# Kernel optimization log

Measured on AMD Instinct MI355X. Metric: run time of the kernel, lower is better.

The kernel has to match this reference:

```python
import jax, jax.numpy as jnp
import numpy as np

EPS_BN = 1e-3   # nn.BatchNorm1d(eps=0.001)
LAMDA = 1e-5    # Point_Attentation.lamda


def _bn(x, g, b, m, v):
    # inference-mode BatchNorm1d over last dim
    return (x - m) * (g * jax.lax.rsqrt(v + EPS_BN)) + b


def _forward(features_low, features_high,
             bott_W, bott_b, bott_gamma, bott_beta, bott_mean, bott_var,
             qkv_W, qkv_gamma, qkv_beta, qkv_mean, qkv_var,
             mlp_W, mlp_gamma, mlp_beta, mlp_mean, mlp_var,
             fus_W, fus_b, fus_gamma, fus_beta, fus_mean, fus_var,
             batch_size):
    N, C = features_low.shape
    B = batch_size
    n = N // B  # points per batch segment (equal-length segments)

    # ---- Point_Attentation: per-point channel mean, var over channels / (n-1) ----
    x = features_low
    mean = jnp.mean(x, axis=-1, keepdims=True)
    d = x - mean
    var = jnp.sum(d * d, axis=-1, keepdims=True) / (n - 1)
    e_t = d * d / (4.0 * (var + LAMDA)) + 0.5
    x = x + jax.nn.sigmoid(e_t) * x

    for i in range(3):
        y = jax.nn.relu(_bn(x @ bott_W[2 * i] + bott_b[2 * i],
                            bott_gamma[2 * i], bott_beta[2 * i], bott_mean[2 * i], bott_var[2 * i]))
        y = jax.nn.relu(_bn(y @ bott_W[2 * i + 1] + bott_b[2 * i + 1],
                            bott_gamma[2 * i + 1], bott_beta[2 * i + 1], bott_mean[2 * i + 1], bott_var[2 * i + 1]))
        x = x + y

    # ---- fusion: per-batch QKV attention between low (x) and high features ----
    low = x.reshape(B, n, C)
    high = features_high.reshape(B, n, C)

    q = _bn(jnp.einsum('bnc,cd->bnd', low, qkv_W[0]), qkv_gamma[0], qkv_beta[0], qkv_mean[0], qkv_var[0])
    k = _bn(jnp.einsum('bnc,cd->bnd', high, qkv_W[1]), qkv_gamma[1], qkv_beta[1], qkv_mean[1], qkv_var[1])
    v = _bn(jnp.einsum('bnc,cd->bnd', high, qkv_W[2]), qkv_gamma[2], qkv_beta[2], qkv_mean[2], qkv_var[2])

    scale = 1.0 / jnp.sqrt(jnp.asarray(256.0, dtype=q.dtype))  # normal_dim = 256
    attn = jax.nn.softmax(jnp.einsum('bqc,bkc->bqk', q, k) * scale, axis=-1)
    ao = jnp.einsum('bqk,bkc->bqc', attn, v)

    # mlp: (Linear no-bias -> BN -> Dropout(eval=id) -> ReLU) x2
    h = jax.nn.relu(_bn(jnp.einsum('bnc,cd->bnd', ao, mlp_W[0]), mlp_gamma[0], mlp_beta[0], mlp_mean[0], mlp_var[0]))
    h = jax.nn.relu(_bn(jnp.einsum('bnc,cd->bnd', h, mlp_W[1]), mlp_gamma[1], mlp_beta[1], mlp_mean[1], mlp_var[1]))

    # linear_fusion: Linear(2C->C, bias) -> BN -> ReLU
    cat = jnp.concatenate([low, h], axis=-1)  # [B, n, 2C]
    out = jax.nn.relu(_bn(jnp.einsum('bnc,cd->bnd', cat, fus_W) + fus_b, fus_gamma, fus_beta, fus_mean, fus_var))
    return out.reshape(N, C)


def setup_inputs() -> dict:
    key = jax.random.key(0)
    ks = jax.random.split(key, 16)
    N, C, B = 16384, 256, 4
    s = 0.05
    d = {}
    d['features_low'] = jax.random.normal(ks[0], (N, C), jnp.float32)
    d['features_high'] = jax.random.normal(ks[1], (N, C), jnp.float32)
    d['bott_W'] = jax.random.normal(ks[2], (6, C, C), jnp.float32) * s
    d['bott_b'] = jnp.zeros((6, C), jnp.float32)
    d['bott_gamma'] = jnp.ones((6, C), jnp.float32)
    d['bott_beta'] = jnp.zeros((6, C), jnp.float32)
    d['bott_mean'] = jnp.zeros((6, C), jnp.float32)
    d['bott_var'] = jnp.ones((6, C), jnp.float32)
    d['qkv_W'] = jax.random.normal(ks[3], (3, C, C), jnp.float32) * s
    d['qkv_gamma'] = jnp.ones((3, C), jnp.float32)
    d['qkv_beta'] = jnp.zeros((3, C), jnp.float32)
    d['qkv_mean'] = jnp.zeros((3, C), jnp.float32)
    d['qkv_var'] = jnp.ones((3, C), jnp.float32)
    d['mlp_W'] = jax.random.normal(ks[4], (2, C, C), jnp.float32) * s
    d['mlp_gamma'] = jnp.ones((2, C), jnp.float32)
    d['mlp_beta'] = jnp.zeros((2, C), jnp.float32)
    d['mlp_mean'] = jnp.zeros((2, C), jnp.float32)
    d['mlp_var'] = jnp.ones((2, C), jnp.float32)
    d['fus_W'] = jax.random.normal(ks[5], (2 * C, C), jnp.float32) * s
    d['fus_b'] = jnp.zeros((C,), jnp.float32)
    d['fus_gamma'] = jnp.ones((C,), jnp.float32)
    d['fus_beta'] = jnp.zeros((C,), jnp.float32)
    d['fus_mean'] = jnp.zeros((C,), jnp.float32)
    d['fus_var'] = jnp.ones((C,), jnp.float32)
    d['batch_size'] = B
    return d


def reference(features_low, features_high,
              bott_W, bott_b, bott_gamma, bott_beta, bott_mean, bott_var,
              qkv_W, qkv_gamma, qkv_beta, qkv_mean, qkv_var,
              mlp_W, mlp_gamma, mlp_beta, mlp_mean, mlp_var,
              fus_W, fus_b, fus_gamma, fus_beta, fus_mean, fus_var,
              batch_size):
    return _forward(features_low, features_high,
                    bott_W, bott_b, bott_gamma, bott_beta, bott_mean, bott_var,
                    qkv_W, qkv_gamma, qkv_beta, qkv_mean, qkv_var,
                    mlp_W, mlp_gamma, mlp_beta, mlp_mean, mlp_var,
                    fus_W, fus_b, fus_gamma, fus_beta, fus_mean, fus_var,
                    batch_size)
```

## Files before the change

kernel.cpp:

```cpp
#include <hip/hip_runtime.h>
#include <cstdint>
#include <cstddef>

typedef float v4f __attribute__((ext_vector_type(4)));
typedef float v2f __attribute__((ext_vector_type(2)));
typedef short v8s __attribute__((ext_vector_type(8)));
typedef unsigned short v4u __attribute__((ext_vector_type(4)));

typedef unsigned short ubf;

#define NPTS 16384
#define CD   256
#define NBAT 4
#define NPB  4096

__device__ __forceinline__ float bf2f(ubf u) {
    union { unsigned u; float f; } c; c.u = ((unsigned)u) << 16; return c.f;
}
__device__ __forceinline__ ubf f2bf(float f) {
    union { float f; unsigned u; } c; c.f = f;
    unsigned u = c.u;
    u += 0x7fffu + ((u >> 16) & 1u);
    return (ubf)(u >> 16);
}

__global__ __launch_bounds__(256) void k_pre(
    const float* __restrict__ low, float* __restrict__ xout,
    const float* __restrict__ bott, const float* __restrict__ qkv,
    const float* __restrict__ mlp, const float* __restrict__ fus,
    ubf* __restrict__ wt) {
    const int bid = blockIdx.x;
    if (bid < 4096) {
        const int lane = threadIdx.x & 63;
        const int row  = bid * 4 + (threadIdx.x >> 6);
        const float* p = low + (size_t)row * CD + lane * 4;
        v4f v = *reinterpret_cast<const v4f*>(p);
        float d[4];
        float s = v[0] + v[1] + v[2] + v[3];
#pragma unroll
        for (int o = 32; o >= 1; o >>= 1) s += __shfl_xor(s, o);
        const float mean = s * (1.0f / 256.0f);
        float ss = 0.f;
#pragma unroll
        for (int i = 0; i < 4; ++i) { d[i] = v[i] - mean; ss += d[i] * d[i]; }
#pragma unroll
        for (int o = 32; o >= 1; o >>= 1) ss += __shfl_xor(ss, o);
        const float var = ss * (1.0f / 4095.0f);
        const float dn  = 1.0f / (4.0f * (var + 1e-5f));
        v4f o;
#pragma unroll
        for (int i = 0; i < 4; ++i) {
            const float e   = d[i] * d[i] * dn + 0.5f;
            const float sig = 1.0f / (1.0f + __expf(-e));
            o[i] = v[i] * (1.0f + sig);
        }
        *reinterpret_cast<v4f*>(xout + (size_t)row * CD + lane * 4) = o;
        return;
    }
    const int bid2 = bid - 4096;
    const int z = bid2 >> 7, r = bid2 & 127;
    const float* src; int K; size_t doff;
    if (z < 6)       { src = bott + (size_t)z * 65536;       K = 256; doff = (size_t)z * 65536; }
    else if (z < 9)  { src = qkv  + (size_t)(z - 6) * 65536; K = 256; doff = (size_t)z * 65536; }
    else if (z < 11) { src = mlp  + (size_t)(z - 9) * 65536; K = 256; doff = (size_t)z * 65536; }
    else             { src = fus;                            K = 512; doff = (size_t)11 * 65536; }
    const int kt = (r >> 3) * 32, nt = (r & 7) * 32;
    if (kt >= K) return;
    __shared__ ubf tile[32][33];
    const int tx = threadIdx.x & 31, ty = threadIdx.x >> 5;
#pragma unroll
    for (int i = 0; i < 4; ++i)
        tile[ty * 4 + i][tx] = f2bf(src[(size_t)(kt + ty * 4 + i) * 256 + nt + tx]);
    __syncthreads();
    ubf* dst = wt + doff;
#pragma unroll
    for (int i = 0; i < 4; ++i)
        dst[(size_t)(nt + ty * 4 + i) * K + kt + tx] = tile[tx][ty * 4 + i];
}

__global__ __launch_bounds__(256) void k_conv1(
    float* __restrict__ xA, const ubf* __restrict__ wT,
    const float* __restrict__ bb, const float* __restrict__ bg,
    const float* __restrict__ bbe, const float* __restrict__ bm_,
    const float* __restrict__ bv) {
    __shared__ __attribute__((aligned(16))) float xls[64 * 256];
    __shared__ __attribute__((aligned(16))) ubf   yls[64 * 256];

    const int lane = threadIdx.x & 63;
    const int w    = threadIdx.x >> 6;
    const int wr = w >> 1, wc = w & 1;
    const int q15 = lane & 15, g = lane >> 4;
    const int bm = blockIdx.x * 64;

    {
        float* xsrcb = xA + (size_t)bm * 256;
#pragma unroll
        for (int it = 0; it < 16; ++it) {
            const int L4 = (it * 256 + w * 64) * 4;
            const int Ll = L4 + lane * 4;
            const int row = Ll >> 8, col = (Ll & 255) ^ ((row & 7) << 3);
            __builtin_amdgcn_global_load_lds(
                (const __attribute__((address_space(1))) unsigned*)(xsrcb + row * 256 + col),
                (__attribute__((address_space(3))) unsigned*)(xls + L4), 16, 0, 0);
        }
    }
    __syncthreads();

    const int r0l = wr * 32 + q15;
#pragma unroll 1
    for (int s = 0; s < 3; ++s) {
        const ubf* W0 = wT + (size_t)(2 * s) * 65536;
        const ubf* W1 = wT + (size_t)(2 * s + 1) * 65536;

        v4f acc[2][8];
#pragma unroll
        for (int i = 0; i < 2; ++i)
#pragma unroll
            for (int j = 0; j < 8; ++j)
#pragma unroll
                for (int r = 0; r < 4; ++r) acc[i][j][r] = 0.f;
        for (int ks = 0; ks < 8; ++ks) {
            const int k0 = ks * 32 + g * 8;
            v8s afr[2], bfr[8];
#pragma unroll
            for (int mi = 0; mi < 2; ++mi) {
                const int row = r0l + mi * 16;
                const float* ap = &xls[row * 256 + (k0 ^ ((row & 7) << 3))];
                v4f a = *reinterpret_cast<const v4f*>(ap);
                v4f b = *reinterpret_cast<const v4f*>(ap + 4);
                v8s t;
#pragma unroll
                for (int j = 0; j < 4; ++j) { t[j] = (short)f2bf(a[j]); t[j + 4] = (short)f2bf(b[j]); }
                afr[mi] = t;
            }
#pragma unroll
            for (int ni = 0; ni < 8; ++ni)
                bfr[ni] = *reinterpret_cast<const v8s*>(W0 + (size_t)(wc * 128 + ni * 16 + q15) * 256 + k0);
#pragma unroll
            for (int mi = 0; mi < 2; ++mi)
#pragma unroll
                for (int ni = 0; ni < 8; ++ni)
                    acc[mi][ni] = __builtin_amdgcn_mfma_f32_16x16x32_bf16(afr[mi], bfr[ni], acc[mi][ni], 0, 0, 0);
        }
#pragma unroll
        for (int ni = 0; ni < 8; ++ni) {
            const int col = wc * 128 + ni * 16 + q15;
            const float sc  = bg[2 * s * 256 + col] * rsqrtf(bv[2 * s * 256 + col] + 1e-3f);
            const float tc  = bbe[2 * s * 256 + col] - bm_[2 * s * 256 + col] * sc;
            const float bia = bb[2 * s * 256 + col];
#pragma unroll
            for (int mi = 0; mi < 2; ++mi)
#pragma unroll
                for (int r = 0; r < 4; ++r) {
                    const int row = wr * 32 + mi * 16 + g * 4 + r;
                    float z = fmaxf((acc[mi][ni][r] + bia) * sc + tc, 0.f);
                    yls[row * 256 + (col ^ ((row & 7) << 3))] = f2bf(z);
                }
        }
        __syncthreads();

#pragma unroll
        for (int i = 0; i < 2; ++i)
#pragma unroll
            for (int j = 0; j < 8; ++j)
#pragma unroll
                for (int r = 0; r < 4; ++r) acc[i][j][r] = 0.f;
        for (int ks = 0; ks < 8; ++ks) {
            const int k0 = ks * 32 + g * 8;
            v8s afr[2], bfr[8];
#pragma unroll
            for (int mi = 0; mi < 2; ++mi) {
                const int row = r0l + mi * 16;
                afr[mi] = *reinterpret_cast<const v8s*>(&yls[row * 256 + (k0 ^ ((row & 7) << 3))]);
            }
#pragma unroll
            for (int ni = 0; ni < 8; ++ni)
                bfr[ni] = *reinterpret_cast<const v8s*>(W1 + (size_t)(wc * 128 + ni * 16 + q15) * 256 + k0);
#pragma unroll
            for (int mi = 0; mi < 2; ++mi)
#pragma unroll
                for (int ni = 0; ni < 8; ++ni)
                    acc[mi][ni] = __builtin_amdgcn_mfma_f32_16x16x32_bf16(afr[mi], bfr[ni], acc[mi][ni], 0, 0, 0);
        }
#pragma unroll
        for (int ni = 0; ni < 8; ++ni) {
            const int col = wc * 128 + ni * 16 + q15;
            const int c1 = (2 * s + 1) * 256 + col;
            const float sc  = bg[c1] * rsqrtf(bv[c1] + 1e-3f);
            const float tc  = bbe[c1] - bm_[c1] * sc;
            const float bia = bb[c1];
#pragma unroll
            for (int mi = 0; mi < 2; ++mi)
#pragma unroll
                for (int r = 0; r < 4; ++r) {
                    const int row = wr * 32 + mi * 16 + g * 4 + r;
                    float z = fmaxf((acc[mi][ni][r] + bia) * sc + tc, 0.f);
                    xls[row * 256 + (col ^ ((row & 7) << 3))] += z;
                }
        }
        __syncthreads();
    }

    {
        float* xdstb = xA + (size_t)bm * 256;
#pragma unroll
        for (int it = 0; it < 16; ++it) {
            const int Ll = (it * 256 + threadIdx.x) * 4;
            const int row = Ll >> 8, cl = Ll & 255;
            const int gcol = cl ^ ((row & 7) << 3);
            *reinterpret_cast<v4f*>(xdstb + row * 256 + gcol) =
                *reinterpret_cast<const v4f*>(xls + Ll);
        }
    }
}

__global__ __launch_bounds__(256) void k_qkv(
    const float* __restrict__ xA, const float* __restrict__ fh,
    const ubf* __restrict__ wTq,
    const float* __restrict__ qg, const float* __restrict__ qbe,
    const float* __restrict__ qm, const float* __restrict__ qv,
    ubf* __restrict__ qB, ubf* __restrict__ kB, ubf* __restrict__ vT) {
    const int m = blockIdx.y >> 1;
    const float* Af = (m == 0) ? xA : fh;
    const ubf* WT = wTq + m * 65536;
    const float* gamma = qg + m * 256;
    const float* beta  = qbe + m * 256;
    const float* bmean = qm + m * 256;
    const float* bvar  = qv + m * 256;

    const int lane = threadIdx.x & 63;
    const int w    = threadIdx.x >> 6;
    const int wr = w >> 1, wc = w & 1;
    const int q15 = lane & 15, g = lane >> 4;
    const int bm = blockIdx.x * 128, bn = (blockIdx.y & 1) * 128;
    const int r0 = bm + wr * 64 + q15;
    const int c0 = bn + wc * 64 + q15;

    v4f acc[4][4];
#pragma unroll
    for (int i = 0; i < 4; ++i)
#pragma unroll
        for (int j = 0; j < 4; ++j)
#pragma unroll
            for (int r = 0; r < 4; ++r) acc[i][j][r] = 0.f;

    for (int ks = 0; ks < 8; ++ks) {
        const int k0 = ks * 32 + g * 8;
        v8s afr[4], bfr[4];
#pragma unroll
        for (int mi = 0; mi < 4; ++mi) {
            const float* ap = Af + (size_t)(r0 + mi * 16) * CD + k0;
            v4f a = *reinterpret_cast<const v4f*>(ap);
            v4f b = *reinterpret_cast<const v4f*>(ap + 4);
            v8s t;
#pragma unroll
            for (int j = 0; j < 4; ++j) { t[j] = (short)f2bf(a[j]); t[j + 4] = (short)f2bf(b[j]); }
            afr[mi] = t;
        }
#pragma unroll
        for (int ni = 0; ni < 4; ++ni)
            bfr[ni] = *reinterpret_cast<const v8s*>(WT + (size_t)(c0 + ni * 16) * 256 + k0);
#pragma unroll
        for (int mi = 0; mi < 4; ++mi)
#pragma unroll
            for (int ni = 0; ni < 4; ++ni)
                acc[mi][ni] = __builtin_amdgcn_mfma_f32_16x16x32_bf16(afr[mi], bfr[ni], acc[mi][ni], 0, 0, 0);
    }

    ubf* outb = (m == 0) ? qB : kB;
#pragma unroll
    for (int ni = 0; ni < 4; ++ni) {
        const int col = c0 + ni * 16;
        const float sc = gamma[col] * rsqrtf(bvar[col] + 1e-3f);
        const float tc = beta[col] - bmean[col] * sc;
#pragma unroll
        for (int mi = 0; mi < 4; ++mi) {
            if (m == 2) {
                const int row0 = bm + wr * 64 + mi * 16 + g * 4;
                v4u pk;
#pragma unroll
                for (int r = 0; r < 4; ++r) pk[r] = f2bf(acc[mi][ni][r] * sc + tc);
                const int bb = row0 >> 12, key = row0 & 4095;
                *reinterpret_cast<v4u*>(vT + ((size_t)(bb * CD + col)) * NPB + key) = pk;
            } else {
#pragma unroll
                for (int r = 0; r < 4; ++r) {
                    const int row = bm + wr * 64 + mi * 16 + g * 4 + r;
                    outb[(size_t)row * CD + col] = f2bf(acc[mi][ni][r] * sc + tc);
                }
            }
        }
    }
}

__device__ __forceinline__ void stage_k32(const ubf* __restrict__ kg,
                                          ubf* kd, int wave, int lane) {
#pragma unroll
    for (int it = 0; it < 8; ++it) {
        const int Lb = it * 1024 + wave * 512;
        const int L  = Lb + lane * 8;
        const int key = L >> 8, c8 = (L & 255) ^ ((key & 7) << 3);
        __builtin_amdgcn_global_load_lds(
            (const __attribute__((address_space(1))) unsigned*)(kg + key * CD + c8),
            (__attribute__((address_space(3))) unsigned*)(kd + Lb), 16, 0, 0);
    }
}
__device__ __forceinline__ void stage_v32(const ubf* __restrict__ vg,
                                          ubf* vd, int wave, int lane) {
#pragma unroll
    for (int it = 0; it < 8; ++it) {
        const int Lb = it * 1024 + wave * 512;
        const int L  = Lb + lane * 8;
        const int cpair = L >> 6;
        const int rem   = (L & 63) ^ ((cpair & 7) << 3);
        const int c = cpair * 2 + (rem >> 5), k = rem & 31;
        __builtin_amdgcn_global_load_lds(
            (const __attribute__((address_space(1))) unsigned*)(vg + (size_t)c * NPB + k),
            (__attribute__((address_space(3))) unsigned*)(vd + Lb), 16, 0, 0);
    }
}

__global__ __launch_bounds__(128, 2) void k_attn(const ubf* __restrict__ qb, const ubf* __restrict__ kb,
                                                 const ubf* __restrict__ vt,
                                                 ubf* __restrict__ o0, ubf* __restrict__ o1,
                                                 float* __restrict__ ml) {
    __shared__ __attribute__((aligned(16))) ubf kls[32 * 256];
    __shared__ __attribute__((aligned(16))) ubf vls[128 * 64];
    __shared__ __attribute__((aligned(16))) ubf pls[2 * 1024];

    const int raw = blockIdx.x;
    const int xcd = raw & 7, qt = raw >> 3;
    const int b = xcd >> 1, half = xcd & 1;

    const int wave = threadIdx.x >> 6, lane = threadIdx.x & 63;
    const int q15 = lane & 15, g = lane >> 4;
    const int swzP = (q15 & 7) << 3;

    const ubf* qrow = qb + ((size_t)(b * NPB + qt * 32 + wave * 16 + q15)) * CD + g * 8;
    v8s qf[8];
#pragma unroll
    for (int cs = 0; cs < 8; ++cs) qf[cs] = *reinterpret_cast<const v8s*>(qrow + cs * 32);

    v4f oacc[16];
#pragma unroll
    for (int i = 0; i < 16; ++i)
#pragma unroll
        for (int r = 0; r < 4; ++r) oacc[i][r] = 0.f;
    float m_run = -3.0e38f, l_run = 0.f;

    const ubf* kgb = kb + ((size_t)(b * NPB) + half * 2048) * CD;
    const ubf* vgb = vt + (size_t)b * CD * NPB + half * 2048;
    ubf* pw = pls + wave * 1024;

    stage_k32(kgb, kls, wave, lane);
    stage_v32(vgb, vls, wave, lane);
    __syncthreads();

    for (int kc = 0; kc < 64; ++kc) {
        v4f sacc[2];
#pragma unroll
        for (int f = 0; f < 2; ++f)
#pragma unroll
            for (int r = 0; r < 4; ++r) sacc[f][r] = 0.f;
#pragma unroll
        for (int cs = 0; cs < 8; ++cs)
#pragma unroll
            for (int f = 0; f < 2; ++f) {
                const int key = 16 * f + q15;
                v8s af = *reinterpret_cast<const v8s*>(&kls[(key * CD + cs * 32 + g * 8) ^ ((key & 7) << 3)]);
                sacc[f] = __builtin_amdgcn_mfma_f32_16x16x32_bf16(af, qf[cs], sacc[f], 0, 0, 0);
            }

        __syncthreads();
        if (kc + 1 < 64)
            stage_k32(kgb + (size_t)(kc + 1) * 32 * CD, kls, wave, lane);

        float mloc = -3.0e38f;
#pragma unroll
        for (int f = 0; f < 2; ++f)
#pragma unroll
            for (int r = 0; r < 4; ++r) {
                float x = sacc[f][r] * 0.0625f;
                sacc[f][r] = x;
                mloc = fmaxf(mloc, x);
            }
        mloc = fmaxf(mloc, __shfl_xor(mloc, 16));
        mloc = fmaxf(mloc, __shfl_xor(mloc, 32));
        if (!__all(mloc <= m_run + 8.0f)) {
            const float mnew  = fmaxf(m_run, mloc);
            const float alpha = __expf(m_run - mnew);
            l_run *= alpha;
#pragma unroll
            for (int i = 0; i < 16; ++i)
#pragma unroll
                for (int r = 0; r < 4; ++r) oacc[i][r] *= alpha;
            m_run = mnew;
        }
        float lloc = 0.f;
#pragma unroll
        for (int f = 0; f < 2; ++f)
#pragma unroll
            for (int r = 0; r < 4; ++r) {
                float p = __expf(sacc[f][r] - m_run);
                sacc[f][r] = p;
                lloc += p;
            }
        lloc += __shfl_xor(lloc, 16);
        lloc += __shfl_xor(lloc, 32);
        l_run += lloc;

#pragma unroll
        for (int f = 0; f < 2; ++f) {
            unsigned u0, u1, u2, u3;
            { union { float f; unsigned u; } c; c.f = sacc[f][0]; u0 = c.u; }
            { union { float f; unsigned u; } c; c.f = sacc[f][1]; u1 = c.u; }
            { union { float f; unsigned u; } c; c.f = sacc[f][2]; u2 = c.u; }
            { union { float f; unsigned u; } c; c.f = sacc[f][3]; u3 = c.u; }
            unsigned p01 = (u0 >> 16) | (u1 & 0xFFFF0000u);
            unsigned p23 = (u2 >> 16) | (u3 & 0xFFFF0000u);
            const int e = q15 * 64 + 16 * f + 4 * g;
            *reinterpret_cast<unsigned*>(&pw[(e)     ^ swzP]) = p01;
            *reinterpret_cast<unsigned*>(&pw[(e + 2) ^ swzP]) = p23;
        }
        v8s pb = *reinterpret_cast<const v8s*>(&pw[(q15 * 64 + 8 * g) ^ swzP]);
#pragma unroll
        for (int mt = 0; mt < 16; ++mt) {
            const int cp = 8 * mt + (q15 >> 1);
            const int e  = cp * 64 + ((((q15 & 1) << 5) | (g << 3)) ^ ((q15 >> 1) << 3));
            v8s av = *reinterpret_cast<const v8s*>(&vls[e]);
            oacc[mt] = __builtin_amdgcn_mfma_f32_16x16x32_bf16(av, pb, oacc[mt], 0, 0, 0);
        }

        __syncthreads();
        if (kc + 1 < 64)
            stage_v32(vgb + (kc + 1) * 32, vls, wave, lane);
    }

    const int grow = b * NPB + qt * 32 + wave * 16 + q15;
    ubf* aor = (half ? o1 : o0) + (size_t)grow * CD;
#pragma unroll
    for (int mt = 0; mt < 16; ++mt) {
        v4u pk;
#pragma unroll
        for (int r = 0; r < 4; ++r) pk[r] = f2bf(oacc[mt][r]);
        *reinterpret_cast<v4u*>(aor + 16 * mt + 4 * g) = pk;
    }
    if (g == 0) {
        v2f d; d[0] = m_run; d[1] = l_run;
        *reinterpret_cast<v2f*>(ml + (size_t)(half * NPTS + grow) * 2) = d;
    }
}

__global__ __launch_bounds__(256) void k_tail(
    const ubf* __restrict__ o0, const ubf* __restrict__ o1, const float* __restrict__ ml,
    const float* __restrict__ xA, const ubf* __restrict__ wT,
    const float* __restrict__ mg, const float* __restrict__ mbe,
    const float* __restrict__ mm, const float* __restrict__ mv,
    const float* __restrict__ fb, const float* __restrict__ fg,
    const float* __restrict__ fbe, const float* __restrict__ fm,
    const float* __restrict__ fv, float* __restrict__ out) {
    __shared__ __attribute__((aligned(16))) ubf yls[64 * 256];

    const int lane = threadIdx.x & 63;
    const int w    = threadIdx.x >> 6;
    const int wr = w >> 1, wc = w & 1;
    const int q15 = lane & 15, g = lane >> 4;
    const int bm = blockIdx.x * 64;
    const int r0l = wr * 32 + q15;

    const ubf* W9  = wT + (size_t)9 * 65536;
    const ubf* W10 = wT + (size_t)10 * 65536;
    const ubf* W11 = wT + (size_t)11 * 65536;

    v4f acc[2][8];

    float a0[2], a1[2];
#pragma unroll
    for (int mi = 0; mi < 2; ++mi) {
        const int row = bm + r0l + mi * 16;
        const float m0 = ml[2 * row],          l0 = ml[2 * row + 1];
        const float m1 = ml[2 * (NPTS + row)], l1 = ml[2 * (NPTS + row) + 1];
        const float mx = fmaxf(m0, m1);
        const float w0 = __expf(m0 - mx), w1 = __expf(m1 - mx);
        const float inv = 1.0f / (w0 * l0 + w1 * l1);
        a0[mi] = w0 * inv; a1[mi] = w1 * inv;
    }
#pragma unroll
    for (int i = 0; i < 2; ++i)
#pragma unroll
        for (int j = 0; j < 8; ++j)
#pragma unroll
            for (int r = 0; r < 4; ++r) acc[i][j][r] = 0.f;
    for (int ks = 0; ks < 8; ++ks) {
        const int k0 = ks * 32 + g * 8;
        v8s afr[2], bfr[8];
#pragma unroll
        for (int mi = 0; mi < 2; ++mi) {
            const int row = bm + r0l + mi * 16;
            v8s u0 = *reinterpret_cast<const v8s*>(o0 + (size_t)row * CD + k0);
            v8s u1 = *reinterpret_cast<const v8s*>(o1 + (size_t)row * CD + k0);
            v8s t;
#pragma unroll
            for (int j = 0; j < 8; ++j)
                t[j] = (short)f2bf(a0[mi] * bf2f((ubf)u0[j]) + a1[mi] * bf2f((ubf)u1[j]));
            afr[mi] = t;
        }
#pragma unroll
        for (int ni = 0; ni < 8; ++ni)
            bfr[ni] = *reinterpret_cast<const v8s*>(W9 + (size_t)(wc * 128 + ni * 16 + q15) * 256 + k0);
#pragma unroll
        for (int mi = 0; mi < 2; ++mi)
#pragma unroll
            for (int ni = 0; ni < 8; ++ni)
                acc[mi][ni] = __builtin_amdgcn_mfma_f32_16x16x32_bf16(afr[mi], bfr[ni], acc[mi][ni], 0, 0, 0);
    }
#pragma unroll
    for (int ni = 0; ni < 8; ++ni) {
        const int col = wc * 128 + ni * 16 + q15;
        const float sc = mg[col] * rsqrtf(mv[col] + 1e-3f);
        const float tc = mbe[col] - mm[col] * sc;
#pragma unroll
        for (int mi = 0; mi < 2; ++mi)
#pragma unroll
            for (int r = 0; r < 4; ++r) {
                const int row = wr * 32 + mi * 16 + g * 4 + r;
                float z = fmaxf(acc[mi][ni][r] * sc + tc, 0.f);
                yls[row * 256 + (col ^ ((row & 7) << 3))] = f2bf(z);
            }
    }
    __syncthreads();

#pragma unroll
    for (int i = 0; i < 2; ++i)
#pragma unroll
        for (int j = 0; j < 8; ++j)
#pragma unroll
            for (int r = 0; r < 4; ++r) acc[i][j][r] = 0.f;
    for (int ks = 0; ks < 8; ++ks) {
        const int k0 = ks * 32 + g * 8;
        v8s afr[2], bfr[8];
#pragma unroll
        for (int mi = 0; mi < 2; ++mi) {
            const int row = r0l + mi * 16;
            afr[mi] = *reinterpret_cast<const v8s*>(&yls[row * 256 + (k0 ^ ((row & 7) << 3))]);
        }
#pragma unroll
        for (int ni = 0; ni < 8; ++ni)
            bfr[ni] = *reinterpret_cast<const v8s*>(W10 + (size_t)(wc * 128 + ni * 16 + q15) * 256 + k0);
#pragma unroll
        for (int mi = 0; mi < 2; ++mi)
#pragma unroll
            for (int ni = 0; ni < 8; ++ni)
                acc[mi][ni] = __builtin_amdgcn_mfma_f32_16x16x32_bf16(afr[mi], bfr[ni], acc[mi][ni], 0, 0, 0);
    }
    __syncthreads();
#pragma unroll
    for (int ni = 0; ni < 8; ++ni) {
        const int col = wc * 128 + ni * 16 + q15;
        const float sc = mg[256 + col] * rsqrtf(mv[256 + col] + 1e-3f);
        const float tc = mbe[256 + col] - mm[256 + col] * sc;
#pragma unroll
        for (int mi = 0; mi < 2; ++mi)
#pragma unroll
            for (int r = 0; r < 4; ++r) {
                const int row = wr * 32 + mi * 16 + g * 4 + r;
                float z = fmaxf(acc[mi][ni][r] * sc + tc, 0.f);
                yls[row * 256 + (col ^ ((row & 7) << 3))] = f2bf(z);
            }
    }
    __syncthreads();

#pragma unroll
    for (int i = 0; i < 2; ++i)
#pragma unroll
        for (int j = 0; j < 8; ++j)
#pragma unroll
            for (int r = 0; r < 4; ++r) acc[i][j][r] = 0.f;
    for (int ks = 0; ks < 16; ++ks) {
        const int k0 = ks * 32 + g * 8;
        v8s afr[2], bfr[8];
#pragma unroll
        for (int mi = 0; mi < 2; ++mi) {
            if (k0 < 256) {
                const float* ap = xA + (size_t)(bm + r0l + mi * 16) * CD + k0;
                v4f a = *reinterpret_cast<const v4f*>(ap);
                v4f b = *reinterpret_cast<const v4f*>(ap + 4);
                v8s t;
#pragma unroll
                for (int j = 0; j < 4; ++j) { t[j] = (short)f2bf(a[j]); t[j + 4] = (short)f2bf(b[j]); }
                afr[mi] = t;
            } else {
                const int row = r0l + mi * 16, kk = k0 - 256;
                afr[mi] = *reinterpret_cast<const v8s*>(&yls[row * 256 + (kk ^ ((row & 7) << 3))]);
            }
        }
#pragma unroll
        for (int ni = 0; ni < 8; ++ni)
            bfr[ni] = *reinterpret_cast<const v8s*>(W11 + (size_t)(wc * 128 + ni * 16 + q15) * 512 + k0);
#pragma unroll
        for (int mi = 0; mi < 2; ++mi)
#pragma unroll
            for (int ni = 0; ni < 8; ++ni)
                acc[mi][ni] = __builtin_amdgcn_mfma_f32_16x16x32_bf16(afr[mi], bfr[ni], acc[mi][ni], 0, 0, 0);
    }
#pragma unroll
    for (int ni = 0; ni < 8; ++ni) {
        const int col = wc * 128 + ni * 16 + q15;
        const float sc = fg[col] * rsqrtf(fv[col] + 1e-3f);
        const float tc = fbe[col] - fm[col] * sc;
        const float bia = fb[col];
#pragma unroll
        for (int mi = 0; mi < 2; ++mi)
#pragma unroll
            for (int r = 0; r < 4; ++r) {
                const int row = bm + wr * 32 + mi * 16 + g * 4 + r;
                float z = fmaxf((acc[mi][ni][r] + bia) * sc + tc, 0.f);
                out[(size_t)row * CD + col] = z;
            }
    }
}

extern "C" void kernel_launch(void* const* d_in, const int* in_sizes, int n_in,
                              void* d_out, int out_size, void* d_ws, size_t ws_size,
                              hipStream_t stream) {
    const float* f_low   = (const float*)d_in[0];
    const float* f_high  = (const float*)d_in[1];
    const float* bott_W  = (const float*)d_in[2];
    const float* bott_b  = (const float*)d_in[3];
    const float* bott_g  = (const float*)d_in[4];
    const float* bott_be = (const float*)d_in[5];
    const float* bott_m  = (const float*)d_in[6];
    const float* bott_v  = (const float*)d_in[7];
    const float* qkv_W   = (const float*)d_in[8];
    const float* qkv_g   = (const float*)d_in[9];
    const float* qkv_be  = (const float*)d_in[10];
    const float* qkv_m   = (const float*)d_in[11];
    const float* qkv_v   = (const float*)d_in[12];
    const float* mlp_W   = (const float*)d_in[13];
    const float* mlp_g   = (const float*)d_in[14];
    const float* mlp_be  = (const float*)d_in[15];
    const float* mlp_m   = (const float*)d_in[16];
    const float* mlp_v   = (const float*)d_in[17];
    const float* fus_W   = (const float*)d_in[18];
    const float* fus_b   = (const float*)d_in[19];
    const float* fus_g   = (const float*)d_in[20];
    const float* fus_be  = (const float*)d_in[21];
    const float* fus_m   = (const float*)d_in[22];
    const float* fus_v   = (const float*)d_in[23];
    (void)in_sizes; (void)n_in; (void)out_size; (void)ws_size;

    char* ws = (char*)d_ws;
    const size_t MB = 1024 * 1024;
    float* xA = (float*)(ws);
    ubf*   o0 = (ubf*)  (ws + 17 * MB);
    ubf*   qB = (ubf*)  (ws + 26 * MB);
    ubf*   kB = (ubf*)  (ws + 35 * MB);
    ubf*   vT = (ubf*)  (ws + 44 * MB);
    ubf*   wT = (ubf*)  (ws + 53 * MB);
    ubf*   o1 = (ubf*)  (ws + 56 * MB);
    float* ml = (float*)(ws + 65 * MB);

    k_pre<<<dim3(4096 + 1536), dim3(256), 0, stream>>>(f_low, xA,
                                                       bott_W, qkv_W, mlp_W, fus_W, wT);

    k_conv1<<<dim3(256), dim3(256), 0, stream>>>(xA, wT,
                                                 bott_b, bott_g, bott_be, bott_m, bott_v);

    k_qkv<<<dim3(128, 6), dim3(256), 0, stream>>>(xA, f_high, wT + (size_t)6 * 65536,
                                                  qkv_g, qkv_be, qkv_m, qkv_v, qB, kB, vT);

    k_attn<<<dim3(1024), dim3(128), 0, stream>>>(qB, kB, vT, o0, o1, ml);

    k_tail<<<dim3(256), dim3(256), 0, stream>>>(o0, o1, ml, xA, wT,
                                                mlp_g, mlp_be, mlp_m, mlp_v,
                                                fus_b, fus_g, fus_be, fus_m, fus_v,
                                                (float*)d_out);
}
```

Before: 305.5 us.

## Switch attention kernel to 32x32x16 MFMA with 64-query tiles and chunked V layout

The flash-attention kernel now uses 32x32x16 bf16 MFMAs with each wave handling 32 queries, so each block covers 64 queries and the grid is halved. This doubles reuse of each staged K/V chunk and cuts K/V LDS traffic per query. V is written in a key-chunked layout (32 keys per channel row) and staged into LDS with a padded 40-element row stride instead of XOR swizzling, and P uses the same padding. The accumulators grow to 128 registers per lane and launch bounds drop to one block per SIMD hint, which lowers occupancy. The padding entries are filled by loading from a dummy address.

```diff
diff --git a/kernel.cpp b/kernel.cpp
--- a/kernel.cpp
+++ b/kernel.cpp
@@ -4,6 +4,7 @@
 
 typedef float v4f __attribute__((ext_vector_type(4)));
 typedef float v2f __attribute__((ext_vector_type(2)));
+typedef float v16f __attribute__((ext_vector_type(16)));
 typedef short v8s __attribute__((ext_vector_type(8)));
 typedef unsigned short v4u __attribute__((ext_vector_type(4)));
 
@@ -281,7 +282,9 @@
 #pragma unroll
                 for (int r = 0; r < 4; ++r) pk[r] = f2bf(acc[mi][ni][r] * sc + tc);
                 const int bb = row0 >> 12, key = row0 & 4095;
-                *reinterpret_cast<v4u*>(vT + ((size_t)(bb * CD + col)) * NPB + key) = pk;
+                const int ch = key >> 5, kin = key & 31;
+                *reinterpret_cast<v4u*>(vT + (size_t)bb * (CD * NPB)
+                                           + (size_t)ch * (CD * 32) + col * 32 + kin) = pk;
             } else {
 #pragma unroll
                 for (int r = 0; r < 4; ++r) {
@@ -305,71 +308,66 @@
             (__attribute__((address_space(3))) unsigned*)(kd + Lb), 16, 0, 0);
     }
 }
-__device__ __forceinline__ void stage_v32(const ubf* __restrict__ vg,
+__device__ __forceinline__ void stage_v40(const ubf* __restrict__ vchunk,
                                           ubf* vd, int wave, int lane) {
 #pragma unroll
-    for (int it = 0; it < 8; ++it) {
-        const int Lb = it * 1024 + wave * 512;
-        const int L  = Lb + lane * 8;
-        const int cpair = L >> 6;
-        const int rem   = (L & 63) ^ ((cpair & 7) << 3);
-        const int c = cpair * 2 + (rem >> 5), k = rem & 31;
+    for (int it = 0; it < 10; ++it) {
+        const int e0b = wave * 5120 + it * 512;
+        const int e0  = e0b + lane * 8;
+        const int c   = e0 / 40;
+        const int k0  = e0 - c * 40;
+        const ubf* src = (k0 < 32) ? (vchunk + c * 32 + k0) : vchunk;
         __builtin_amdgcn_global_load_lds(
-            (const __attribute__((address_space(1))) unsigned*)(vg + (size_t)c * NPB + k),
-            (__attribute__((address_space(3))) unsigned*)(vd + Lb), 16, 0, 0);
-    }
-}
-
-__global__ __launch_bounds__(128, 2) void k_attn(const ubf* __restrict__ qb, const ubf* __restrict__ kb,
+            (const __attribute__((address_space(1))) unsigned*)src,
+            (__attribute__((address_space(3))) unsigned*)(vd + e0b), 16, 0, 0);
+    }
+}
+
+__global__ __launch_bounds__(128, 1) void k_attn(const ubf* __restrict__ qb, const ubf* __restrict__ kb,
                                                  const ubf* __restrict__ vt,
                                                  ubf* __restrict__ o0, ubf* __restrict__ o1,
                                                  float* __restrict__ ml) {
     __shared__ __attribute__((aligned(16))) ubf kls[32 * 256];
-    __shared__ __attribute__((aligned(16))) ubf vls[128 * 64];
-    __shared__ __attribute__((aligned(16))) ubf pls[2 * 1024];
+    __shared__ __attribute__((aligned(16))) ubf vls[256 * 40];
+    __shared__ __attribute__((aligned(16))) ubf pls[2 * 32 * 40];
 
     const int raw = blockIdx.x;
     const int xcd = raw & 7, qt = raw >> 3;
     const int b = xcd >> 1, half = xcd & 1;
 
     const int wave = threadIdx.x >> 6, lane = threadIdx.x & 63;
-    const int q15 = lane & 15, g = lane >> 4;
-    const int swzP = (q15 & 7) << 3;
-
-    const ubf* qrow = qb + ((size_t)(b * NPB + qt * 32 + wave * 16 + q15)) * CD + g * 8;
-    v8s qf[8];
-#pragma unroll
-    for (int cs = 0; cs < 8; ++cs) qf[cs] = *reinterpret_cast<const v8s*>(qrow + cs * 32);
-
-    v4f oacc[16];
-#pragma unroll
-    for (int i = 0; i < 16; ++i)
-#pragma unroll
-        for (int r = 0; r < 4; ++r) oacc[i][r] = 0.f;
+    const int q31 = lane & 31, h = lane >> 5;
+
+    const ubf* qrow = qb + ((size_t)(b * NPB + qt * 64 + wave * 32 + q31)) * CD + h * 8;
+    v8s qf[16];
+#pragma unroll
+    for (int ks = 0; ks < 16; ++ks) qf[ks] = *reinterpret_cast<const v8s*>(qrow + ks * 16);
+
+    v16f oacc[8];
+#pragma unroll
+    for (int t = 0; t < 8; ++t)
+#pragma unroll
+        for (int r = 0; r < 16; ++r) oacc[t][r] = 0.f;
     float m_run = -3.0e38f, l_run = 0.f;
 
     const ubf* kgb = kb + ((size_t)(b * NPB) + half * 2048) * CD;
-    const ubf* vgb = vt + (size_t)b * CD * NPB + half * 2048;
-    ubf* pw = pls + wave * 1024;
+    const ubf* vgb = vt + (size_t)b * (CD * NPB) + (size_t)(half * 64) * (CD * 32);
+    ubf* pw = pls + wave * (32 * 40);
 
     stage_k32(kgb, kls, wave, lane);
-    stage_v32(vgb, vls, wave, lane);
+    stage_v40(vgb, vls, wave, lane);
     __syncthreads();
 
     for (int kc = 0; kc < 64; ++kc) {
-        v4f sacc[2];
-#pragma unroll
-        for (int f = 0; f < 2; ++f)
-#pragma unroll
-            for (int r = 0; r < 4; ++r) sacc[f][r] = 0.f;
-#pragma unroll
-        for (int cs = 0; cs < 8; ++cs)
-#pragma unroll
-            for (int f = 0; f < 2; ++f) {
-                const int key = 16 * f + q15;
-                v8s af = *reinterpret_cast<const v8s*>(&kls[(key * CD + cs * 32 + g * 8) ^ ((key & 7) << 3)]);
-                sacc[f] = __builtin_amdgcn_mfma_f32_16x16x32_bf16(af, qf[cs], sacc[f], 0, 0, 0);
-            }
+        v16f sacc;
+#pragma unroll
+        for (int r = 0; r < 16; ++r) sacc[r] = 0.f;
+#pragma unroll
+        for (int ks = 0; ks < 16; ++ks) {
+            v8s af = *reinterpret_cast<const v8s*>(
+                &kls[q31 * 256 + ((ks * 16 + h * 8) ^ ((q31 & 7) << 3))]);
+            sacc = __builtin_amdgcn_mfma_f32_32x32x16_bf16(af, qf[ks], sacc, 0, 0, 0);
+        }
 
         __syncthreads();
         if (kc + 1 < 64)
@@ -377,75 +375,73 @@
 
         float mloc = -3.0e38f;
 #pragma unroll
-        for (int f = 0; f < 2; ++f)
-#pragma unroll
-            for (int r = 0; r < 4; ++r) {
-                float x = sacc[f][r] * 0.0625f;
-                sacc[f][r] = x;
-                mloc = fmaxf(mloc, x);
-            }
-        mloc = fmaxf(mloc, __shfl_xor(mloc, 16));
+        for (int r = 0; r < 16; ++r) {
+            float x = sacc[r] * 0.0625f;
+            sacc[r] = x;
+            mloc = fmaxf(mloc, x);
+        }
         mloc = fmaxf(mloc, __shfl_xor(mloc, 32));
         if (!__all(mloc <= m_run + 8.0f)) {
             const float mnew  = fmaxf(m_run, mloc);
             const float alpha = __expf(m_run - mnew);
             l_run *= alpha;
 #pragma unroll
-            for (int i = 0; i < 16; ++i)
-#pragma unroll
-                for (int r = 0; r < 4; ++r) oacc[i][r] *= alpha;
+            for (int t = 0; t < 8; ++t)
+#pragma unroll
+                for (int r = 0; r < 16; ++r) oacc[t][r] *= alpha;
             m_run = mnew;
         }
         float lloc = 0.f;
 #pragma unroll
-        for (int f = 0; f < 2; ++f)
-#pragma unroll
-            for (int r = 0; r < 4; ++r) {
-                float p = __expf(sacc[f][r] - m_run);
-                sacc[f][r] = p;
-                lloc += p;
-            }
-        lloc += __shfl_xor(lloc, 16);
+        for (int r = 0; r < 16; ++r) {
+            float p = __expf(sacc[r] - m_run);
+            sacc[r] = p;
+            lloc += p;
+        }
         lloc += __shfl_xor(lloc, 32);
         l_run += lloc;
 
 #pragma unroll
-        for (int f = 0; f < 2; ++f) {
+        for (int G = 0; G < 4; ++G) {
             unsigned u0, u1, u2, u3;
-            { union { float f; unsigned u; } c; c.f = sacc[f][0]; u0 = c.u; }
-            { union { float f; unsigned u; } c; c.f = sacc[f][1]; u1 = c.u; }
-            { union { float f; unsigned u; } c; c.f = sacc[f][2]; u2 = c.u; }
-            { union { float f; unsigned u; } c; c.f = sacc[f][3]; u3 = c.u; }
+            { union { float f; unsigned u; } c; c.f = sacc[4 * G + 0]; u0 = c.u; }
+            { union { float f; unsigned u; } c; c.f = sacc[4 * G + 1]; u1 = c.u; }
+            { union { float f; unsigned u; } c; c.f = sacc[4 * G + 2]; u2 = c.u; }
+            { union { float f; unsigned u; } c; c.f = sacc[4 * G + 3]; u3 = c.u; }
             unsigned p01 = (u0 >> 16) | (u1 & 0xFFFF0000u);
             unsigned p23 = (u2 >> 16) | (u3 & 0xFFFF0000u);
-            const int e = q15 * 64 + 16 * f + 4 * g;
-            *reinterpret_cast<unsigned*>(&pw[(e)     ^ swzP]) = p01;
-            *reinterpret_cast<unsigned*>(&pw[(e + 2) ^ swzP]) = p23;
-        }
-        v8s pb = *reinterpret_cast<const v8s*>(&pw[(q15 * 64 + 8 * g) ^ swzP]);
-#pragma unroll
-        for (int mt = 0; mt < 16; ++mt) {
-            const int cp = 8 * mt + (q15 >> 1);
-            const int e  = cp * 64 + ((((q15 & 1) << 5) | (g << 3)) ^ ((q15 >> 1) << 3));
-            v8s av = *reinterpret_cast<const v8s*>(&vls[e]);
-            oacc[mt] = __builtin_amdgcn_mfma_f32_16x16x32_bf16(av, pb, oacc[mt], 0, 0, 0);
+            const int e = q31 * 40 + 8 * G + 4 * h;
+            *reinterpret_cast<unsigned*>(&pw[e])     = p01;
+            *reinterpret_cast<unsigned*>(&pw[e + 2]) = p23;
+        }
+        v8s pb0 = *reinterpret_cast<const v8s*>(&pw[q31 * 40 + 0  + 8 * h]);
+        v8s pb1 = *reinterpret_cast<const v8s*>(&pw[q31 * 40 + 16 + 8 * h]);
+#pragma unroll
+        for (int t = 0; t < 8; ++t) {
+            const int crow = (t * 32 + q31) * 40;
+            v8s av0 = *reinterpret_cast<const v8s*>(&vls[crow + 0  + 8 * h]);
+            oacc[t] = __builtin_amdgcn_mfma_f32_32x32x16_bf16(av0, pb0, oacc[t], 0, 0, 0);
+            v8s av1 = *reinterpret_cast<const v8s*>(&vls[crow + 16 + 8 * h]);
+            oacc[t] = __builtin_amdgcn_mfma_f32_32x32x16_bf16(av1, pb1, oacc[t], 0, 0, 0);
         }
 
         __syncthreads();
         if (kc + 1 < 64)
-            stage_v32(vgb + (kc + 1) * 32, vls, wave, lane);
-    }
-
-    const int grow = b * NPB + qt * 32 + wave * 16 + q15;
+            stage_v40(vgb + (size_t)(kc + 1) * (CD * 32), vls, wave, lane);
+    }
+
+    const int grow = b * NPB + qt * 64 + wave * 32 + q31;
     ubf* aor = (half ? o1 : o0) + (size_t)grow * CD;
 #pragma unroll
-    for (int mt = 0; mt < 16; ++mt) {
-        v4u pk;
-#pragma unroll
-        for (int r = 0; r < 4; ++r) pk[r] = f2bf(oacc[mt][r]);
-        *reinterpret_cast<v4u*>(aor + 16 * mt + 4 * g) = pk;
-    }
-    if (g == 0) {
+    for (int t = 0; t < 8; ++t)
+#pragma unroll
+        for (int G = 0; G < 4; ++G) {
+            v4u pk;
+#pragma unroll
+            for (int r = 0; r < 4; ++r) pk[r] = f2bf(oacc[t][4 * G + r]);
+            *reinterpret_cast<v4u*>(aor + t * 32 + 8 * G + 4 * h) = pk;
+        }
+    if (h == 0) {
         v2f d; d[0] = m_run; d[1] = l_run;
         *reinterpret_cast<v2f*>(ml + (size_t)(half * NPTS + grow) * 2) = d;
     }
@@ -669,7 +665,7 @@
     k_qkv<<<dim3(128, 6), dim3(256), 0, stream>>>(xA, f_high, wT + (size_t)6 * 65536,
                                                   qkv_g, qkv_be, qkv_m, qkv_v, qB, kB, vT);
 
-    k_attn<<<dim3(1024), dim3(128), 0, stream>>>(qB, kB, vT, o0, o1, ml);
+    k_attn<<<dim3(512), dim3(128), 0, stream>>>(qB, kB, vT, o0, o1, ml);
 
     k_tail<<<dim3(256), dim3(256), 0, stream>>>(o0, o1, ml, xA, wT,
                                                 mlp_g, mlp_be, mlp_m, mlp_v,
```

Measured after the change: 287.1 us. -6.0%, faster.
